# Kernel optimization log

Measured on AMD Instinct MI355X. Metric: run time of the kernel, lower is better.

## Reference

```python
import jax, jax.numpy as jnp
import numpy as np

NUM_CLASSES = 81
OUTPUT_SIZE = 19
NMS_THRESH = 0.45
TOP_K = 400          # pre-NMS candidates per class == max_output_size of tf NMS
KEEP_TOP_K = 200
CONF_THRESH = 0.01
MASK_CONF_THRESH = 0.6
B = 8
P = 24564


def setup_inputs() -> dict:
    key = jax.random.key(0)
    k1, k2, k3, k4 = jax.random.split(key, 4)
    # structured x = [loc | conf | priorbox | variances] so the decode math is realistic
    loc = 0.1 * jax.random.normal(k1, (B, P, 4), dtype=jnp.float32)
    conf = jax.random.uniform(k2, (B, P, NUM_CLASSES), dtype=jnp.float32)
    cxcy = jax.random.uniform(k3, (P, 2), minval=0.05, maxval=0.95)
    wh = jax.random.uniform(k4, (P, 2), minval=0.05, maxval=0.3)
    pmin = jnp.clip(cxcy - 0.5 * wh, 0.0, 1.0)
    pmax = jnp.clip(cxcy + 0.5 * wh, 0.0, 1.0)
    priors = jnp.broadcast_to(jnp.concatenate([pmin, pmax], -1), (B, P, 4)).astype(jnp.float32)
    variances = jnp.full((B, P, 4), 0.1, dtype=jnp.float32)
    x = jnp.concatenate([loc, conf, priors, variances], -1)
    return {"x": x}


def decode_boxes(loc, prior, var):
    pw = prior[..., 2] - prior[..., 0]
    ph = prior[..., 3] - prior[..., 1]
    pcx = 0.5 * (prior[..., 2] + prior[..., 0])
    pcy = 0.5 * (prior[..., 3] + prior[..., 1])
    cx = loc[..., 0] * pw * var[..., 0] + pcx
    cy = loc[..., 1] * pw * var[..., 1] + pcy  # uses prior_width, faithful to original code
    w = jnp.exp(loc[..., 2] * var[..., 2]) * pw
    h = jnp.exp(loc[..., 3] * var[..., 3]) * ph
    box = jnp.stack([cx - 0.5 * w, cy - 0.5 * h, cx + 0.5 * w, cy + 0.5 * h], -1)
    return jnp.clip(box, 0.0, 1.0)


def iou_matrix(b):  # [N,4] xyxy -> [N,N]
    area = (b[:, 2] - b[:, 0]) * (b[:, 3] - b[:, 1])
    ix1 = jnp.maximum(b[:, None, 0], b[None, :, 0])
    iy1 = jnp.maximum(b[:, None, 1], b[None, :, 1])
    ix2 = jnp.minimum(b[:, None, 2], b[None, :, 2])
    iy2 = jnp.minimum(b[:, None, 3], b[None, :, 3])
    inter = jnp.maximum(ix2 - ix1, 0.0) * jnp.maximum(iy2 - iy1, 0.0)
    union = area[:, None] + area[None, :] - inter
    return jnp.where(union > 0.0, inter / union, 0.0)


def greedy_nms(iou, valid):  # candidates already sorted desc by score
    n = valid.shape[0]
    def body(kept, i):
        sup = jnp.any(kept & (iou[i] > NMS_THRESH))
        return kept.at[i].set(valid[i] & ~sup), None
    kept, _ = jax.lax.scan(body, jnp.zeros(n, dtype=bool), jnp.arange(n))
    return kept


def _forward(x):
    b = x.shape[0]
    loc = x[..., :4]
    conf = x[..., 4:4 + NUM_CLASSES]
    prior = x[..., -8:-4]
    var = x[..., -4:]
    boxes = decode_boxes(loc, prior, var)                        # [B,P,4]
    cls_conf = jnp.swapaxes(conf[..., 1:], 1, 2)                 # [B,C-1,P] (skip background class 0)
    masked = jnp.where(cls_conf > CONF_THRESH, cls_conf, -1.0)
    scores, idx = jax.lax.top_k(masked, TOP_K)                   # [B,C-1,K]
    cand = jnp.take_along_axis(boxes[:, None], idx[..., None], axis=2)  # [B,C-1,K,4]
    valid = scores > CONF_THRESH
    iou = jax.vmap(jax.vmap(iou_matrix))(cand)                   # [B,C-1,K,K]
    kept = jax.vmap(jax.vmap(greedy_nms))(iou, valid)            # [B,C-1,K]
    labels = jnp.broadcast_to(jnp.arange(1, NUM_CLASSES)[None, :, None], scores.shape)
    det_scores = jnp.where(kept, scores, -1.0).reshape(b, -1)
    det_boxes = cand.reshape(b, -1, 4)
    det_labels = labels.reshape(b, -1)
    order = jnp.argsort(-det_scores, axis=1)[:, :KEEP_TOP_K]     # sort desc by conf, keep_top_k=200
    top_s = jnp.take_along_axis(det_scores, order, 1)            # [B,200]
    top_b = jnp.take_along_axis(det_boxes, order[..., None], 1)  # [B,200,4]
    top_l = jnp.take_along_axis(det_labels, order, 1)            # [B,200]

    def rasterize(s, bx, lb):
        vld = s >= MASK_CONF_THRESH
        co = jnp.round(bx * OUTPUT_SIZE).astype(jnp.int32)       # [K,4] x1,y1,x2,y2
        g = jnp.arange(OUTPUT_SIZE)
        cover = ((g[None, :, None] >= co[:, 1, None, None]) & (g[None, :, None] < co[:, 3, None, None]) &
                 (g[None, None, :] >= co[:, 0, None, None]) & (g[None, None, :] < co[:, 2, None, None]) &
                 vld[:, None, None])                             # [K,S,S]
        chan = lb - 1                                            # label-1 channel, as in original
        kidx = jnp.arange(KEEP_TOP_K)
        def per_channel(c):
            cov = cover & (chan == c)[:, None, None]
            win = jnp.max(jnp.where(cov, kidx[:, None, None], -1), axis=0)  # [S,S]
            return jnp.where(win >= 0, s[jnp.clip(win, 0)], 0.0)
        return jnp.transpose(jax.vmap(per_channel)(jnp.arange(NUM_CLASSES)), (1, 2, 0))

    return jax.vmap(rasterize)(top_s, top_b, top_l)              # [B,S,S,C]


def reference(x):
    return _forward(x)
```

## Files before the change

### kernel.cpp

```cpp
#include <hip/hip_runtime.h>

#define NB 8
#define NP 24564
#define NCLS 80
#define TOPK 400
#define KEEPK 200
#define OUTS 19
#define NCELL (OUTS * OUTS)
#define DETN (NCLS * TOPK)
#define CKS 32008
#define ROWS 64
#define CHUNKS ((NP + ROWS - 1) / ROWS)
#define CAP 1024
#define T0 0.972f
#define NT 512
#define LCAP 16
#define CSTR 16

__device__ __forceinline__ unsigned f2ord(float f) {
    unsigned u = __float_as_uint(f);
    return (u & 0x80000000u) ? ~u : (u | 0x80000000u);
}
__device__ __forceinline__ float ord2f(unsigned k) {
    unsigned u = (k & 0x80000000u) ? (k & 0x7fffffffu) : ~k;
    return __uint_as_float(u);
}
__device__ __forceinline__ unsigned bin16(unsigned key) {
    int b = (int)(key >> 16) - 0xBC00;
    b = b < 0 ? 0 : (b > 1023 ? 1023 : b);
    return (unsigned)b;
}

__device__ __forceinline__ void bitonic_desc(unsigned long long* cand, unsigned S, int tid) {
    for (unsigned k = 2; k <= S; k <<= 1)
        for (unsigned j = k >> 1; j; j >>= 1) {
            for (unsigned i = tid; i < S; i += NT) {
                unsigned l = i ^ j;
                if (l > i) {
                    unsigned long long a = cand[i], bq = cand[l];
                    bool sw = ((i & k) == 0) ? (a < bq) : (a > bq);
                    if (sw) { cand[i] = bq; cand[l] = a; }
                }
            }
            __syncthreads();
        }
}

__global__ __launch_bounds__(256) void kZ(unsigned long long* __restrict__ ckeys,
                                          unsigned* __restrict__ ccnt,
                                          unsigned* __restrict__ gflag,
                                          unsigned* __restrict__ kcnt) {
    int t = blockIdx.x * 256 + threadIdx.x;
    for (int i = t; i < NB * CKS; i += gridDim.x * 256) ckeys[i] = 0ull;
    for (int i = t; i < NB * NCLS * CSTR; i += gridDim.x * 256) ccnt[i] = 0u;
    if (t < NB * NCLS) gflag[t] = 0u;
    if (t < NB * 16) kcnt[t] = 0u;
}

__global__ __launch_bounds__(NT) void kA(const float* __restrict__ x,
                                         float4* __restrict__ boxes,
                                         unsigned long long* __restrict__ pcand,
                                         unsigned* __restrict__ ccnt,
                                         unsigned* __restrict__ gflag) {
    __shared__ float tile[ROWS * 93];
    __shared__ unsigned long long list[NCLS * LCAP];
    __shared__ unsigned lcnt[NCLS];
    __shared__ unsigned lbase[NCLS];

    int blk = blockIdx.x;
    int b = blk / CHUNKS, chunk = blk % CHUNKS;
    int p0 = chunk * ROWS;
    int nrows = NP - p0; if (nrows > ROWS) nrows = ROWS;
    const float* src = x + (size_t)(b * NP + p0) * 93;
    int total4 = (nrows * 93) >> 2;
    const float4* s4 = (const float4*)src;
    float4* t4 = (float4*)tile;
    for (int e = threadIdx.x; e < total4; e += NT) t4[e] = s4[e];
    __syncthreads();

    int row = threadIdx.x & 63;
    int lane = row;
    int cg = threadIdx.x >> 6;
    unsigned p = (unsigned)(p0 + row);
    bool rowOk = row < nrows;
    for (int c = cg; c < NCLS; c += (NT / 64)) {
        float v = rowOk ? tile[row * 93 + 5 + c] : -1.0f;
        bool pred = v > T0;
        unsigned long long bal = __ballot(pred);
        if (pred) {
            unsigned rank = (unsigned)__popcll(bal & ((1ull << lane) - 1ull));
            if (rank < LCAP)
                list[c * LCAP + rank] =
                    ((unsigned long long)f2ord(v) << 32) | (unsigned)(~p);
        }
        if (lane == 0) lcnt[c] = (unsigned)__popcll(bal);
    }

    if (threadIdx.x < nrows) {
        const float* r = tile + threadIdx.x * 93;
        float l0 = r[0], l1 = r[1], l2 = r[2], l3 = r[3];
        float px1 = r[85], py1 = r[86], px2 = r[87], py2 = r[88];
        float v0 = r[89], v1 = r[90], v2 = r[91], v3 = r[92];
        float pw = px2 - px1, ph = py2 - py1;
        float pcx = 0.5f * (px2 + px1), pcy = 0.5f * (py2 + py1);
        float cx = l0 * pw * v0 + pcx;
        float cy = l1 * pw * v1 + pcy;
        float w = expf(l2 * v2) * pw;
        float h = expf(l3 * v3) * ph;
        float x1 = fminf(fmaxf(cx - 0.5f * w, 0.f), 1.f);
        float y1 = fminf(fmaxf(cy - 0.5f * h, 0.f), 1.f);
        float x2 = fminf(fmaxf(cx + 0.5f * w, 0.f), 1.f);
        float y2 = fminf(fmaxf(cy + 0.5f * h, 0.f), 1.f);
        boxes[(size_t)b * NP + p0 + threadIdx.x] = make_float4(x1, y1, x2, y2);
    }
    __syncthreads();

    if (threadIdx.x < NCLS) {
        unsigned n = lcnt[threadIdx.x];
        unsigned wr = (n > LCAP) ? LCAP : n;
        lbase[threadIdx.x] =
            wr ? atomicAdd(&ccnt[(b * NCLS + threadIdx.x) * CSTR], wr) : 0u;
        lcnt[threadIdx.x] = wr;
        if (n > LCAP) gflag[b * NCLS + threadIdx.x] = 1u;
    }
    __syncthreads();

    for (int idx = threadIdx.x; idx < NCLS * LCAP; idx += NT) {
        int c = idx >> 4, i = idx & (LCAP - 1);
        if ((unsigned)i < lcnt[c]) {
            unsigned pos = lbase[c] + (unsigned)i;
            if (pos < CAP)
                pcand[((size_t)(b * NCLS + c) << 10) + pos] = list[idx];
        }
    }
}

__device__ void select_strided(const float* __restrict__ src, unsigned needed,
                               unsigned long long* cand,
                               unsigned* hist, unsigned* aux, unsigned* scal,
                               int tid) {
    for (int i = tid; i < 1024; i += NT) hist[i] = 0u;
    if (tid == 0) { scal[0] = 0u; scal[1] = 0u; scal[2] = 0u; scal[3] = 0u; }
    __syncthreads();
    for (int p = tid; p < NP; p += NT) {
        float v = src[(size_t)p * 93];
        float m = (v > 0.01f) ? v : -1.0f;
        atomicAdd(&hist[bin16(f2ord(m))], 1u);
    }
    __syncthreads();
    unsigned h0 = 0, h1 = 0, h2 = 0, h3 = 0;
    if (tid < 256) {
        h0 = hist[4 * tid]; h1 = hist[4 * tid + 1];
        h2 = hist[4 * tid + 2]; h3 = hist[4 * tid + 3];
        aux[tid] = h0 + h1 + h2 + h3;
    }
    __syncthreads();
    for (int d = 1; d < 256; d <<= 1) {
        unsigned v = 0u;
        if (tid < 256 && tid + d < 256) v = aux[tid + d];
        __syncthreads();
        if (tid < 256) aux[tid] += v;
        __syncthreads();
    }
    if (tid < 256) {
        unsigned above = (tid < 255) ? aux[tid + 1] : 0u;
        unsigned s3 = above + h3, s2 = s3 + h2, s1 = s2 + h1, s0 = s1 + h0;
        if (s0 >= needed && s1 < needed) { scal[0] = 4 * tid;     scal[1] = s1;    scal[2] = s0; }
        if (s1 >= needed && s2 < needed) { scal[0] = 4 * tid + 1; scal[1] = s2;    scal[2] = s1; }
        if (s2 >= needed && s3 < needed) { scal[0] = 4 * tid + 2; scal[1] = s3;    scal[2] = s2; }
        if (s3 >= needed && above < needed) { scal[0] = 4 * tid + 3; scal[1] = above; scal[2] = s3; }
    }
    __syncthreads();
    unsigned cb = scal[0], countHigh = scal[1], countAt = scal[2];
    unsigned cut8 = 0;
    if (countAt > CAP) {
        if (tid < 256) aux[tid] = 0u;
        __syncthreads();
        for (int p = tid; p < NP; p += NT) {
            float v = src[(size_t)p * 93];
            float m = (v > 0.01f) ? v : -1.0f;
            unsigned k = f2ord(m);
            if (bin16(k) == cb) atomicAdd(&aux[(k >> 8) & 255u], 1u);
        }
        __syncthreads();
        for (int d = 1; d < 256; d <<= 1) {
            unsigned v = 0u;
            if (tid < 256 && tid + d < 256) v = aux[tid + d];
            __syncthreads();
            if (tid < 256) aux[tid] += v;
            __syncthreads();
        }
        if (tid < 256) {
            unsigned suf8 = aux[tid];
            unsigned sufN = (tid < 255) ? aux[tid + 1] : 0u;
            unsigned need2 = needed - countHigh;
            if (suf8 >= need2 && sufN < need2) scal[3] = (unsigned)tid;
        }
        __syncthreads();
        cut8 = scal[3];
    }
    __syncthreads();
    if (tid == 0) scal[1] = 0u;
    __syncthreads();
    for (int p = tid; p < NP; p += NT) {
        float v = src[(size_t)p * 93];
        float m = (v > 0.01f) ? v : -1.0f;
        unsigned key = f2ord(m);
        unsigned b16 = bin16(key);
        bool take = (b16 > cb) || (b16 == cb && ((key >> 8) & 255u) >= cut8);
        if (take) {
            unsigned pos = atomicAdd(&scal[1], 1u);
            if (pos < CAP) cand[pos] = ((unsigned long long)key << 32) | (unsigned)(~p);
        }
    }
    __syncthreads();
    unsigned cc = scal[1]; if (cc > CAP) cc = CAP;
    for (unsigned i = tid; i < CAP; i += NT) if (i >= cc) cand[i] = 0ull;
    __syncthreads();
    bitonic_desc(cand, (cc <= 512u) ? 512u : (unsigned)CAP, tid);
}

struct HistU { unsigned hist[1024]; unsigned aux[256]; };
union SelU { HistU s; unsigned iouRow[TOPK][13]; };

__global__ __launch_bounds__(NT) void kNms(const float* __restrict__ x,
                                           const float4* __restrict__ boxes,
                                           const unsigned long long* __restrict__ pcand,
                                           const unsigned* __restrict__ ccnt,
                                           const unsigned* __restrict__ gflag,
                                           unsigned long long* __restrict__ ckeys,
                                           float4* __restrict__ cboxes,
                                           unsigned* __restrict__ kcnt) {
    __shared__ unsigned long long cand[CAP];
    __shared__ float4 selBox[TOPK];
    __shared__ float selArea[TOPK];
    __shared__ unsigned scal[4];
    __shared__ SelU U;
    __shared__ unsigned keptWords[13];

    int b = blockIdx.x / NCLS, c = blockIdx.x % NCLS;
    int tid = threadIdx.x;

    unsigned count = ccnt[(b * NCLS + c) * CSTR];
    const unsigned long long* src = pcand + ((size_t)(b * NCLS + c) << 10);
    bool fast = (gflag[b * NCLS + c] == 0u) && (count >= TOPK) && (count <= CAP);
    if (fast) {
        for (unsigned i = tid; i < CAP; i += NT) cand[i] = (i < count) ? src[i] : 0ull;
        __syncthreads();
        bitonic_desc(cand, (count <= 512u) ? 512u : (unsigned)CAP, tid);
    } else {
        select_strided(x + (size_t)b * NP * 93 + 5 + c, TOPK,
                       cand, U.s.hist, U.s.aux, scal, tid);
    }

    for (int k = tid; k < TOPK; k += NT) {
        unsigned idx = ~(unsigned)cand[k];
        if (idx >= NP) idx = 0;
        float4 bx = boxes[(size_t)b * NP + idx];
        selBox[k] = bx;
        selArea[k] = (bx.z - bx.x) * (bx.w - bx.y);
    }
    __syncthreads();

    {
        int r = tid;
        if (r < TOPK) {
            float4 br = selBox[r];
            float ar = selArea[r];
            int nw = (r >> 5) + 1;
            for (int w = 0; w < nw; ++w) {
                unsigned word = 0;
#pragma unroll 8
                for (int jj = 0; jj < 32; ++jj) {
                    int j = w * 32 + jj;
                    float4 bj = selBox[j];
                    float ix = fminf(br.z, bj.z) - fmaxf(br.x, bj.x);
                    float iy = fminf(br.w, bj.w) - fmaxf(br.y, bj.y);
                    float inter = fmaxf(ix, 0.f) * fmaxf(iy, 0.f);
                    float uni = ar + selArea[j] - inter;
                    word |= (unsigned)(inter > 0.45f * uni) << jj;
                }
                U.iouRow[r][w] = word;
            }
        }
    }
    __syncthreads();

    if (tid < 64) {
        unsigned lane = tid;
        unsigned myKept = 0;
        const unsigned VALID_KEY = f2ord(0.01f);
        unsigned w = (lane < 13) ? U.iouRow[0][lane] : 0u;
        for (int i = 0; i < TOPK; ++i) {
            unsigned wn = (i < TOPK - 1 && lane < 13) ? U.iouRow[i + 1][lane] : 0u;
            bool hit = (w & myKept) != 0u;
            unsigned long long bal = __ballot(hit);
            unsigned keyi = (unsigned)(cand[i] >> 32);
            bool kept = (keyi > VALID_KEY) && (bal == 0ull);
            if (kept && lane == (unsigned)(i >> 5)) myKept |= 1u << (i & 31);
            w = wn;
        }
        if (lane < 13) keptWords[lane] = myKept;
    }
    __syncthreads();

    if (tid == 0) {
        unsigned total = 0;
        for (int w = 0; w < 13; ++w) total += __popc(keptWords[w]);
        scal[2] = atomicAdd(&kcnt[b * 16], total);
    }
    __syncthreads();
    unsigned base = scal[2];
    size_t kb = (size_t)b * CKS;
    size_t bb = (size_t)b * DETN;
    for (int k = tid; k < TOPK; k += NT) {
        unsigned flat = (unsigned)(c * TOPK + k);
        cboxes[bb + flat] = selBox[k];
        bool kept = (keptWords[k >> 5] >> (k & 31)) & 1u;
        if (kept) {
            unsigned rank = 0;
            int wi = k >> 5;
            for (int w = 0; w < wi; ++w) rank += __popc(keptWords[w]);
            rank += __popc(keptWords[wi] & ((1u << (k & 31)) - 1u));
            unsigned key = (unsigned)(cand[k] >> 32);
            ckeys[kb + base + rank] = ((unsigned long long)key << 32) | (unsigned)(~flat);
        }
    }
}

__global__ __launch_bounds__(NT) void kC(const unsigned long long* __restrict__ ckeys,
                                         const float4* __restrict__ cboxes,
                                         const unsigned* __restrict__ kcnt,
                                         float* __restrict__ out) {
    __shared__ unsigned long long cand[CAP];
    __shared__ HistU S;
    __shared__ unsigned scal[4];
    __shared__ float eS[KEEPK];
    __shared__ int eC0[KEEPK], eC1[KEEPK], eC2[KEEPK], eC3[KEEPK];
    __shared__ int eCh[KEEPK];

    int b = blockIdx.x;
    int tid = threadIdx.x;
    const ulonglong2* k2 = (const ulonglong2*)(ckeys + (size_t)b * CKS);
    int n = (int)kcnt[b * 16]; if (n > DETN) n = DETN;
    int n2 = (n + 1) >> 1;
    const unsigned needed = KEEPK;

    for (int i = tid; i < 1024; i += NT) S.hist[i] = 0u;
    if (tid == 0) { scal[0] = 0u; scal[1] = 0u; scal[2] = 0u; scal[3] = 0u; }
    __syncthreads();
    for (int i = tid; i < n2; i += NT) {
        ulonglong2 v = k2[i];
        atomicAdd(&S.hist[bin16((unsigned)(v.x >> 32))], 1u);
        atomicAdd(&S.hist[bin16((unsigned)(v.y >> 32))], 1u);
    }
    __syncthreads();
    unsigned h0 = 0, h1 = 0, h2 = 0, h3 = 0;
    if (tid < 256) {
        h0 = S.hist[4 * tid]; h1 = S.hist[4 * tid + 1];
        h2 = S.hist[4 * tid + 2]; h3 = S.hist[4 * tid + 3];
        S.aux[tid] = h0 + h1 + h2 + h3;
    }
    __syncthreads();
    for (int d = 1; d < 256; d <<= 1) {
        unsigned v = 0u;
        if (tid < 256 && tid + d < 256) v = S.aux[tid + d];
        __syncthreads();
        if (tid < 256) S.aux[tid] += v;
        __syncthreads();
    }
    if (tid < 256) {
        unsigned above = (tid < 255) ? S.aux[tid + 1] : 0u;
        unsigned s3 = above + h3, s2 = s3 + h2, s1 = s2 + h1, s0 = s1 + h0;
        if (s0 >= needed && s1 < needed) { scal[0] = 4 * tid;     scal[1] = s1;    scal[2] = s0; }
        if (s1 >= needed && s2 < needed) { scal[0] = 4 * tid + 1; scal[1] = s2;    scal[2] = s1; }
        if (s2 >= needed && s3 < needed) { scal[0] = 4 * tid + 2; scal[1] = s3;    scal[2] = s2; }
        if (s3 >= needed && above < needed) { scal[0] = 4 * tid + 3; scal[1] = above; scal[2] = s3; }
    }
    __syncthreads();
    unsigned cb = scal[0], countHigh = scal[1], countAt = scal[2];
    unsigned cut8 = 0;
    if (countAt > CAP) {
        if (tid < 256) S.aux[tid] = 0u;
        __syncthreads();
        for (int i = tid; i < n2; i += NT) {
            ulonglong2 v = k2[i];
            unsigned kx = (unsigned)(v.x >> 32), ky = (unsigned)(v.y >> 32);
            if (bin16(kx) == cb) atomicAdd(&S.aux[(kx >> 8) & 255u], 1u);
            if (bin16(ky) == cb) atomicAdd(&S.aux[(ky >> 8) & 255u], 1u);
        }
        __syncthreads();
        for (int d = 1; d < 256; d <<= 1) {
            unsigned v = 0u;
            if (tid < 256 && tid + d < 256) v = S.aux[tid + d];
            __syncthreads();
            if (tid < 256) S.aux[tid] += v;
            __syncthreads();
        }
        if (tid < 256) {
            unsigned suf8 = S.aux[tid];
            unsigned sufN = (tid < 255) ? S.aux[tid + 1] : 0u;
            unsigned need2 = needed - countHigh;
            if (suf8 >= need2 && sufN < need2) scal[3] = (unsigned)tid;
        }
        __syncthreads();
        cut8 = scal[3];
    }
    __syncthreads();
    if (tid == 0) scal[1] = 0u;
    __syncthreads();
    for (int i = tid; i < n2; i += NT) {
        ulonglong2 v = k2[i];
#pragma unroll
        for (int c = 0; c < 2; ++c) {
            unsigned long long key = c ? v.y : v.x;
            unsigned kh = (unsigned)(key >> 32);
            unsigned b16 = bin16(kh);
            bool take = (b16 > cb) || (b16 == cb && ((kh >> 8) & 255u) >= cut8);
            if (take) {
                unsigned pos = atomicAdd(&scal[1], 1u);
                if (pos < CAP) cand[pos] = key;
            }
        }
    }
    __syncthreads();
    unsigned cc = scal[1]; if (cc > CAP) cc = CAP;
    for (unsigned i = tid; i < CAP; i += NT) if (i >= cc) cand[i] = 0ull;
    __syncthreads();
    bitonic_desc(cand, (cc <= 512u) ? 512u : (unsigned)CAP, tid);

    for (int k = tid; k < KEEPK; k += NT) {
        unsigned long long K = cand[k];
        unsigned key = (unsigned)(K >> 32);
        unsigned flat = ~(unsigned)K;
        if (flat >= DETN) flat = 0;
        float4 bx = cboxes[(size_t)b * DETN + flat];
        eS[k] = (key == 0u) ? -1.0f : ord2f(key);
        eC0[k] = (int)rintf(bx.x * (float)OUTS);
        eC1[k] = (int)rintf(bx.y * (float)OUTS);
        eC2[k] = (int)rintf(bx.z * (float)OUTS);
        eC3[k] = (int)rintf(bx.w * (float)OUTS);
        eCh[k] = (int)(flat / TOPK);
    }
    __syncthreads();

    for (int cell = tid; cell < NCELL; cell += NT) {
        int y = cell / OUTS, x = cell % OUTS;
        float* o = out + ((size_t)b * NCELL + cell) * 81;
        for (int ch = 0; ch < 81; ++ch) o[ch] = 0.f;
        for (int k = 0; k < KEEPK; ++k) {
            float s = eS[k];
            if (s < 0.6f) continue;
            if (y >= eC1[k] && y < eC3[k] && x >= eC0[k] && x < eC2[k])
                o[eCh[k]] = s;
        }
    }
}

extern "C" void kernel_launch(void* const* d_in, const int* in_sizes, int n_in,
                              void* d_out, int out_size, void* d_ws, size_t ws_size,
                              hipStream_t stream) {
    const float* x = (const float*)d_in[0];
    float* out = (float*)d_out;

    float4* boxes   = (float4*)d_ws;
    float4* cboxes  = boxes + (size_t)NB * NP;
    unsigned long long* ckeys = (unsigned long long*)(cboxes + (size_t)NB * DETN);
    unsigned long long* pcand = ckeys + (size_t)NB * CKS;
    unsigned* ccnt = (unsigned*)(pcand + ((size_t)NB * NCLS << 10));
    unsigned* gflag = ccnt + NB * NCLS * CSTR;
    unsigned* kcnt  = gflag + NB * NCLS;

    kZ<<<256, 256, 0, stream>>>(ckeys, ccnt, gflag, kcnt);
    kA<<<NB * CHUNKS, NT, 0, stream>>>(x, boxes, pcand, ccnt, gflag);
    kNms<<<NB * NCLS, NT, 0, stream>>>(x, boxes, pcand, ccnt, gflag, ckeys, cboxes, kcnt);
    kC<<<NB, NT, 0, stream>>>(ckeys, cboxes, kcnt, out);
}
```

Before: 287.5 us.

## Sort candidates in registers with shuffles and pack triangular IoU work

Replaces the shared-memory bitonic sort in the NMS and final-select kernels with a register-resident 1024-element bitonic sort. Strides of 64 or less use warp shuffles and only the wider strides go through shared memory. The IoU bitmask build is rewritten as a flat list of packed lower-triangle word tasks spread over all threads, where before each row was one thread with a varying amount of work. The zero-fill of the ckeys buffer is dropped, and kC now bounds-checks the odd tail element instead of relying on that zeroing. This is meant to cut sync-heavy shared-memory sorting, load imbalance and the memset, at the cost of more register pressure and an index calculation per IoU task.

```diff
diff --git a/kernel.cpp b/kernel.cpp
--- a/kernel.cpp
+++ b/kernel.cpp
@@ -16,6 +16,7 @@
 #define NT 512
 #define LCAP 16
 #define CSTR 16
+#define WTASK 2704
 
 __device__ __forceinline__ unsigned f2ord(float f) {
     unsigned u = __float_as_uint(f);
@@ -29,6 +30,46 @@
     int b = (int)(key >> 16) - 0xBC00;
     b = b < 0 ? 0 : (b > 1023 ? 1023 : b);
     return (unsigned)b;
+}
+
+__device__ __forceinline__ unsigned long long shfl_xor_u64(unsigned long long v, int mask) {
+    unsigned lo = (unsigned)__shfl_xor((int)(unsigned)v, mask);
+    unsigned hi = (unsigned)__shfl_xor((int)(v >> 32), mask);
+    return ((unsigned long long)hi << 32) | lo;
+}
+
+__device__ __forceinline__ void regsort1024(unsigned long long& a0, unsigned long long& a1,
+                                            unsigned long long* sc, unsigned t) {
+    const unsigned e0 = 2u * t;
+#pragma unroll
+    for (unsigned k = 2; k <= 1024; k <<= 1) {
+#pragma unroll
+        for (unsigned j = k >> 1; j >= 128; j >>= 1) {
+            sc[e0] = a0; sc[e0 + 1] = a1;
+            __syncthreads();
+            unsigned p0 = e0 ^ j;
+            unsigned long long b0 = sc[p0], b1 = sc[p0 + 1];
+            bool km = ((e0 & k) == 0u) ^ ((e0 & j) != 0u);
+            a0 = km ? (a0 > b0 ? a0 : b0) : (a0 < b0 ? a0 : b0);
+            a1 = km ? (a1 > b1 ? a1 : b1) : (a1 < b1 ? a1 : b1);
+            __syncthreads();
+        }
+#pragma unroll
+        for (unsigned j = ((k >> 1) < 64u ? (k >> 1) : 64u); j >= 2; j >>= 1) {
+            unsigned long long b0 = shfl_xor_u64(a0, (int)(j >> 1));
+            unsigned long long b1 = shfl_xor_u64(a1, (int)(j >> 1));
+            bool km = ((e0 & k) == 0u) ^ ((e0 & j) != 0u);
+            a0 = km ? (a0 > b0 ? a0 : b0) : (a0 < b0 ? a0 : b0);
+            a1 = km ? (a1 > b1 ? a1 : b1) : (a1 < b1 ? a1 : b1);
+        }
+        {
+            bool dir = ((e0 & k) == 0u);
+            unsigned long long mx = a0 > a1 ? a0 : a1;
+            unsigned long long mn = a0 > a1 ? a1 : a0;
+            a0 = dir ? mx : mn;
+            a1 = dir ? mn : mx;
+        }
+    }
 }
 
 __device__ __forceinline__ void bitonic_desc(unsigned long long* cand, unsigned S, int tid) {
@@ -46,12 +87,10 @@
         }
 }
 
-__global__ __launch_bounds__(256) void kZ(unsigned long long* __restrict__ ckeys,
-                                          unsigned* __restrict__ ccnt,
+__global__ __launch_bounds__(256) void kZ(unsigned* __restrict__ ccnt,
                                           unsigned* __restrict__ gflag,
                                           unsigned* __restrict__ kcnt) {
     int t = blockIdx.x * 256 + threadIdx.x;
-    for (int i = t; i < NB * CKS; i += gridDim.x * 256) ckeys[i] = 0ull;
     for (int i = t; i < NB * NCLS * CSTR; i += gridDim.x * 256) ccnt[i] = 0u;
     if (t < NB * NCLS) gflag[t] = 0u;
     if (t < NB * 16) kcnt[t] = 0u;
@@ -220,8 +259,11 @@
     bitonic_desc(cand, (cc <= 512u) ? 512u : (unsigned)CAP, tid);
 }
 
-struct HistU { unsigned hist[1024]; unsigned aux[256]; };
-union SelU { HistU s; unsigned iouRow[TOPK][13]; };
+union ScratchU {
+    unsigned long long sc[1024];
+    unsigned iouRowP[WTASK];
+    struct { unsigned long long cand[CAP]; unsigned hist[1024]; unsigned aux[256]; } fb;
+};
 
 __global__ __launch_bounds__(NT) void kNms(const float* __restrict__ x,
                                            const float4* __restrict__ boxes,
@@ -231,74 +273,88 @@
                                            unsigned long long* __restrict__ ckeys,
                                            float4* __restrict__ cboxes,
                                            unsigned* __restrict__ kcnt) {
-    __shared__ unsigned long long cand[CAP];
+    __shared__ ScratchU U;
     __shared__ float4 selBox[TOPK];
     __shared__ float selArea[TOPK];
+    __shared__ unsigned selKey[TOPK];
     __shared__ unsigned scal[4];
-    __shared__ SelU U;
     __shared__ unsigned keptWords[13];
 
     int b = blockIdx.x / NCLS, c = blockIdx.x % NCLS;
     int tid = threadIdx.x;
+    unsigned t = (unsigned)tid;
 
     unsigned count = ccnt[(b * NCLS + c) * CSTR];
-    const unsigned long long* src = pcand + ((size_t)(b * NCLS + c) << 10);
     bool fast = (gflag[b * NCLS + c] == 0u) && (count >= TOPK) && (count <= CAP);
+    unsigned long long a0, a1;
     if (fast) {
-        for (unsigned i = tid; i < CAP; i += NT) cand[i] = (i < count) ? src[i] : 0ull;
-        __syncthreads();
-        bitonic_desc(cand, (count <= 512u) ? 512u : (unsigned)CAP, tid);
+        const ulonglong2* src2 =
+            (const ulonglong2*)(pcand + ((size_t)(b * NCLS + c) << 10));
+        ulonglong2 vv = src2[t];
+        a0 = (2u * t     < count) ? vv.x : 0ull;
+        a1 = (2u * t + 1 < count) ? vv.y : 0ull;
+        regsort1024(a0, a1, U.sc, t);
     } else {
         select_strided(x + (size_t)b * NP * 93 + 5 + c, TOPK,
-                       cand, U.s.hist, U.s.aux, scal, tid);
-    }
-
-    for (int k = tid; k < TOPK; k += NT) {
-        unsigned idx = ~(unsigned)cand[k];
-        if (idx >= NP) idx = 0;
-        float4 bx = boxes[(size_t)b * NP + idx];
-        selBox[k] = bx;
-        selArea[k] = (bx.z - bx.x) * (bx.w - bx.y);
-    }
-    __syncthreads();
-
-    {
-        int r = tid;
-        if (r < TOPK) {
-            float4 br = selBox[r];
-            float ar = selArea[r];
-            int nw = (r >> 5) + 1;
-            for (int w = 0; w < nw; ++w) {
-                unsigned word = 0;
+                       U.fb.cand, U.fb.hist, U.fb.aux, scal, tid);
+        a0 = U.fb.cand[2u * t];
+        a1 = U.fb.cand[2u * t + 1];
+    }
+    if (t < TOPK / 2) {
+        unsigned i0 = ~(unsigned)a0; if (i0 >= NP) i0 = 0;
+        unsigned i1 = ~(unsigned)a1; if (i1 >= NP) i1 = 0;
+        float4 b0 = boxes[(size_t)b * NP + i0];
+        float4 b1 = boxes[(size_t)b * NP + i1];
+        selBox[2u * t] = b0;            selBox[2u * t + 1] = b1;
+        selArea[2u * t] = (b0.z - b0.x) * (b0.w - b0.y);
+        selArea[2u * t + 1] = (b1.z - b1.x) * (b1.w - b1.y);
+        selKey[2u * t] = (unsigned)(a0 >> 32);
+        selKey[2u * t + 1] = (unsigned)(a1 >> 32);
+    }
+    __syncthreads();
+
+    for (int T = tid; T < WTASK; T += NT) {
+        int b0i = (int)(sqrtf((float)T * 0.0625f + 0.25f) - 0.5f);
+        while (16 * (b0i + 1) * (b0i + 2) <= T) ++b0i;
+        while (b0i > 0 && 16 * b0i * (b0i + 1) > T) --b0i;
+        int off = T - 16 * b0i * (b0i + 1);
+        int rr = off / (b0i + 1);
+        int w = off - rr * (b0i + 1);
+        int r = 32 * b0i + rr;
+        float4 br = selBox[r];
+        float ar = selArea[r];
+        unsigned word = 0;
 #pragma unroll 8
-                for (int jj = 0; jj < 32; ++jj) {
-                    int j = w * 32 + jj;
-                    float4 bj = selBox[j];
-                    float ix = fminf(br.z, bj.z) - fmaxf(br.x, bj.x);
-                    float iy = fminf(br.w, bj.w) - fmaxf(br.y, bj.y);
-                    float inter = fmaxf(ix, 0.f) * fmaxf(iy, 0.f);
-                    float uni = ar + selArea[j] - inter;
-                    word |= (unsigned)(inter > 0.45f * uni) << jj;
-                }
-                U.iouRow[r][w] = word;
-            }
-        }
+        for (int jj = 0; jj < 32; ++jj) {
+            int j = w * 32 + jj;
+            float4 bj = selBox[j];
+            float ix = fminf(br.z, bj.z) - fmaxf(br.x, bj.x);
+            float iy = fminf(br.w, bj.w) - fmaxf(br.y, bj.y);
+            float inter = fmaxf(ix, 0.f) * fmaxf(iy, 0.f);
+            float uni = ar + selArea[j] - inter;
+            word |= (unsigned)(inter > 0.45f * uni) << jj;
+        }
+        U.iouRowP[T] = word;
     }
     __syncthreads();
 
     if (tid < 64) {
-        unsigned lane = tid;
+        unsigned lane = t;
         unsigned myKept = 0;
         const unsigned VALID_KEY = f2ord(0.01f);
-        unsigned w = (lane < 13) ? U.iouRow[0][lane] : 0u;
+        unsigned ro = 0;
+        unsigned w = (lane < 1u) ? U.iouRowP[lane] : 0u;
         for (int i = 0; i < TOPK; ++i) {
-            unsigned wn = (i < TOPK - 1 && lane < 13) ? U.iouRow[i + 1][lane] : 0u;
+            unsigned nwi = (unsigned)(i >> 5) + 1u;
+            unsigned ron = ro + nwi;
+            unsigned wn = 0u;
+            if (i < TOPK - 1 && lane <= (unsigned)((i + 1) >> 5))
+                wn = U.iouRowP[ron + lane];
             bool hit = (w & myKept) != 0u;
             unsigned long long bal = __ballot(hit);
-            unsigned keyi = (unsigned)(cand[i] >> 32);
-            bool kept = (keyi > VALID_KEY) && (bal == 0ull);
+            bool kept = (selKey[i] > VALID_KEY) && (bal == 0ull);
             if (kept && lane == (unsigned)(i >> 5)) myKept |= 1u << (i & 31);
-            w = wn;
+            w = wn; ro = ron;
         }
         if (lane < 13) keptWords[lane] = myKept;
     }
@@ -322,17 +378,20 @@
             int wi = k >> 5;
             for (int w = 0; w < wi; ++w) rank += __popc(keptWords[w]);
             rank += __popc(keptWords[wi] & ((1u << (k & 31)) - 1u));
-            unsigned key = (unsigned)(cand[k] >> 32);
-            ckeys[kb + base + rank] = ((unsigned long long)key << 32) | (unsigned)(~flat);
-        }
-    }
-}
+            ckeys[kb + base + rank] =
+                ((unsigned long long)selKey[k] << 32) | (unsigned)(~flat);
+        }
+    }
+}
+
+struct HistU { unsigned hist[1024]; unsigned aux[256]; };
 
 __global__ __launch_bounds__(NT) void kC(const unsigned long long* __restrict__ ckeys,
                                          const float4* __restrict__ cboxes,
                                          const unsigned* __restrict__ kcnt,
                                          float* __restrict__ out) {
     __shared__ unsigned long long cand[CAP];
+    __shared__ unsigned long long scK[CAP];
     __shared__ HistU S;
     __shared__ unsigned scal[4];
     __shared__ float eS[KEEPK];
@@ -341,6 +400,7 @@
 
     int b = blockIdx.x;
     int tid = threadIdx.x;
+    unsigned t = (unsigned)tid;
     const ulonglong2* k2 = (const ulonglong2*)(ckeys + (size_t)b * CKS);
     int n = (int)kcnt[b * 16]; if (n > DETN) n = DETN;
     int n2 = (n + 1) >> 1;
@@ -352,7 +412,7 @@
     for (int i = tid; i < n2; i += NT) {
         ulonglong2 v = k2[i];
         atomicAdd(&S.hist[bin16((unsigned)(v.x >> 32))], 1u);
-        atomicAdd(&S.hist[bin16((unsigned)(v.y >> 32))], 1u);
+        if (2 * i + 1 < n) atomicAdd(&S.hist[bin16((unsigned)(v.y >> 32))], 1u);
     }
     __syncthreads();
     unsigned h0 = 0, h1 = 0, h2 = 0, h3 = 0;
@@ -387,7 +447,7 @@
             ulonglong2 v = k2[i];
             unsigned kx = (unsigned)(v.x >> 32), ky = (unsigned)(v.y >> 32);
             if (bin16(kx) == cb) atomicAdd(&S.aux[(kx >> 8) & 255u], 1u);
-            if (bin16(ky) == cb) atomicAdd(&S.aux[(ky >> 8) & 255u], 1u);
+            if (2 * i + 1 < n && bin16(ky) == cb) atomicAdd(&S.aux[(ky >> 8) & 255u], 1u);
         }
         __syncthreads();
         for (int d = 1; d < 256; d <<= 1) {
@@ -413,6 +473,7 @@
         ulonglong2 v = k2[i];
 #pragma unroll
         for (int c = 0; c < 2; ++c) {
+            if (c && 2 * i + 1 >= n) continue;
             unsigned long long key = c ? v.y : v.x;
             unsigned kh = (unsigned)(key >> 32);
             unsigned b16 = bin16(kh);
@@ -427,20 +488,26 @@
     unsigned cc = scal[1]; if (cc > CAP) cc = CAP;
     for (unsigned i = tid; i < CAP; i += NT) if (i >= cc) cand[i] = 0ull;
     __syncthreads();
-    bitonic_desc(cand, (cc <= 512u) ? 512u : (unsigned)CAP, tid);
-
-    for (int k = tid; k < KEEPK; k += NT) {
-        unsigned long long K = cand[k];
-        unsigned key = (unsigned)(K >> 32);
-        unsigned flat = ~(unsigned)K;
-        if (flat >= DETN) flat = 0;
-        float4 bx = cboxes[(size_t)b * DETN + flat];
-        eS[k] = (key == 0u) ? -1.0f : ord2f(key);
-        eC0[k] = (int)rintf(bx.x * (float)OUTS);
-        eC1[k] = (int)rintf(bx.y * (float)OUTS);
-        eC2[k] = (int)rintf(bx.z * (float)OUTS);
-        eC3[k] = (int)rintf(bx.w * (float)OUTS);
-        eCh[k] = (int)(flat / TOPK);
+    unsigned long long a0 = cand[2u * t], a1 = cand[2u * t + 1];
+    __syncthreads();
+    regsort1024(a0, a1, scK, t);
+
+    if (t < KEEPK / 2) {
+#pragma unroll
+        for (int q = 0; q < 2; ++q) {
+            unsigned long long K = q ? a1 : a0;
+            unsigned k = 2u * t + q;
+            unsigned key = (unsigned)(K >> 32);
+            unsigned flat = ~(unsigned)K;
+            if (flat >= DETN) flat = 0;
+            float4 bx = cboxes[(size_t)b * DETN + flat];
+            eS[k] = (key == 0u) ? -1.0f : ord2f(key);
+            eC0[k] = (int)rintf(bx.x * (float)OUTS);
+            eC1[k] = (int)rintf(bx.y * (float)OUTS);
+            eC2[k] = (int)rintf(bx.z * (float)OUTS);
+            eC3[k] = (int)rintf(bx.w * (float)OUTS);
+            eCh[k] = (int)(flat / TOPK);
+        }
     }
     __syncthreads();
 
@@ -471,7 +538,7 @@
     unsigned* gflag = ccnt + NB * NCLS * CSTR;
     unsigned* kcnt  = gflag + NB * NCLS;
 
-    kZ<<<256, 256, 0, stream>>>(ckeys, ccnt, gflag, kcnt);
+    kZ<<<40, 256, 0, stream>>>(ccnt, gflag, kcnt);
     kA<<<NB * CHUNKS, NT, 0, stream>>>(x, boxes, pcand, ccnt, gflag);
     kNms<<<NB * NCLS, NT, 0, stream>>>(x, boxes, pcand, ccnt, gflag, ckeys, cboxes, kcnt);
     kC<<<NB, NT, 0, stream>>>(ckeys, cboxes, kcnt, out);
```

Result: faster. 279.8 us (-2.7%).
